# Kernel tuning notes

Hardware: AMD Instinct MI355X
Metric: run time of the kernel (lower is better)

Reference implementation:

```python
import jax, jax.numpy as jnp
import numpy as np

B, D, L = 2, 1024, 4096   # batch, channels (= num_heads), seq len
FS = 4                    # filter_size
DEPTH = 11                # ceil(log2((L-1)/(FS-1)+1))
LN_EPS = 1e-5


def setup_inputs() -> dict:
    key = jax.random.key(0)
    ks = jax.random.split(key, 7)
    return {
        "x": jax.random.normal(ks[0], (B, D, L), jnp.float32),
        "h0": jax.random.normal(ks[1], (D, 1, FS), jnp.float32) * 0.2,
        "h1": jax.random.normal(ks[2], (D, 1, FS), jnp.float32) * 0.2,
        "w_mix": jax.random.normal(ks[3], (D, D), jnp.float32) / np.sqrt(D),
        "b_mix": jnp.zeros((D,), jnp.float32),
        "ln_gamma": jnp.ones((D,), jnp.float32),
        "ln_beta": jnp.zeros((D,), jnp.float32),
    }


def _dw_conv(a, h, dilation):
    # depthwise (groups = D) dilated conv1d, cross-correlation like torch
    return jax.lax.conv_general_dilated(
        a, h, window_strides=(1,), padding='VALID',
        rhs_dilation=(dilation,),
        dimension_numbers=('NCH', 'OIH', 'NCH'),
        feature_group_count=D)


def reference(x, h0, h1, w_mix, b_mix, ln_gamma, ln_beta):
    # --- multires conv tree ---
    a = x
    dilation = 1
    a_list, b_list = [], []
    for _ in range(DEPTH):
        pad = dilation * (FS - 1)
        ap = jnp.pad(a, ((0, 0), (0, 0), (pad, 0)))  # left causal pad
        b = _dw_conv(ap, h1, dilation)
        a = _dw_conv(ap, h0, dilation)
        a_list.append(a)
        b_list.append(b)
        dilation *= 2
    # --- gated combination across scales (deepest level first) ---
    a_rev = a_list[::-1]
    b_rev = b_list[::-1]
    y = jnp.zeros_like(x)
    gated = None
    for i in range(DEPTH):
        if i + 1 < DEPTH:
            gated = jax.nn.sigmoid(a_rev[i]) * b_rev[i + 1]
        # last iteration reuses the previous gated tensor (matches original)
        y = y + gated
    # --- 1x1 channel mix (Dropout1d is identity in eval) + residual ---
    mixed = jnp.einsum('oc,bcl->bol', w_mix, y) + b_mix[None, :, None]
    z = mixed + x
    # --- LayerNorm over channel dim ---
    mu = jnp.mean(z, axis=1, keepdims=True)
    var = jnp.mean(jnp.square(z - mu), axis=1, keepdims=True)
    out = (z - mu) * jax.lax.rsqrt(var + LN_EPS)
    out = out * ln_gamma[None, :, None] + ln_beta[None, :, None]
    return out
```

## Files before the change

### kernel.cpp

```cpp
#include <hip/hip_runtime.h>
#include <hip/hip_bf16.h>

#define NB 2
#define ND 1024
#define NL 4096
#define NFS 4
#define NDEPTH 11
#define LN_EPS 1e-5f

#define BM 128
#define BN 128
#define BK 32
#define NKI (ND / BK)
#define ASZ (BM * BK)

#define CPAD 3072
#define CBUF (CPAD + NL)

typedef __bf16 bf16x8 __attribute__((ext_vector_type(8)));
typedef float f32x4 __attribute__((ext_vector_type(4)));

__device__ __forceinline__ unsigned short f2bf(float f) {
    __hip_bfloat16 h = __float2bfloat16(f);
    unsigned short u;
    __builtin_memcpy(&u, &h, 2);
    return u;
}

__device__ __forceinline__ float bf2f(unsigned short u) {
    unsigned int ui = (unsigned int)u << 16;
    float f;
    __builtin_memcpy(&f, &ui, 4);
    return f;
}

__device__ __forceinline__ unsigned int pack2bf(float lo, float hi) {
    return (unsigned int)f2bf(lo) | ((unsigned int)f2bf(hi) << 16);
}

__device__ __forceinline__ float sigm(float v) {
    return __builtin_amdgcn_rcpf(1.f + __expf(-v));
}

__device__ __forceinline__ void llds16(const void* g, void* l) {
    __builtin_amdgcn_global_load_lds(
        (const __attribute__((address_space(1))) unsigned int*)g,
        (__attribute__((address_space(3))) unsigned int*)l, 16, 0, 0);
}

__global__ __launch_bounds__(256) void wconv_kernel(const float* __restrict__ w,
                                                    unsigned short* __restrict__ wbf) {
    const int idx8 = (blockIdx.x * 256 + threadIdx.x) * 8;
    const float4 v0 = *reinterpret_cast<const float4*>(w + idx8);
    const float4 v1 = *reinterpret_cast<const float4*>(w + idx8 + 4);
    uint4 o;
    o.x = pack2bf(v0.x, v0.y);
    o.y = pack2bf(v0.z, v0.w);
    o.z = pack2bf(v1.x, v1.y);
    o.w = pack2bf(v1.z, v1.w);
    *reinterpret_cast<uint4*>(wbf + idx8) = o;
}

__global__ __launch_bounds__(512, 8) void conv_cascade_kernel(const float* __restrict__ x,
                                                              const float* __restrict__ h0,
                                                              const float* __restrict__ h1,
                                                              unsigned short* __restrict__ ybf) {
    __shared__ float a_sh[CBUF];
    const int row = blockIdx.x;
    const int d = row & (ND - 1);
    const int t = threadIdx.x;

#pragma unroll
    for (int i = 0; i < CPAD / 512; ++i) a_sh[i * 512 + t] = 0.f;

    const float* xrow = x + (size_t)row * NL;

    float h0c[NFS], h1c[NFS];
#pragma unroll
    for (int k = 0; k < NFS; ++k) {
        h0c[k] = h0[d * NFS + k];
        h1c[k] = h1[d * NFS + k];
    }

    float cur[2][4], yacc[2][4], bprev[2][4];
#pragma unroll
    for (int c = 0; c < 2; ++c) {
        const float4 v = *reinterpret_cast<const float4*>(xrow + c * 2048 + t * 4);
        cur[c][0] = v.x; cur[c][1] = v.y; cur[c][2] = v.z; cur[c][3] = v.w;
        *reinterpret_cast<float4*>(&a_sh[CPAD + c * 2048 + t * 4]) = v;
#pragma unroll
        for (int j = 0; j < 4; ++j) { yacc[c][j] = 0.f; bprev[c][j] = 0.f; }
    }
    __syncthreads();

#define CONV_MATH(c, A1, A2, A3, an, bn)                                             \
    _Pragma("unroll") for (int j = 0; j < 4; ++j) {                                  \
        an[j] = h0c[3] * cur[c][j] + h0c[2] * (A1)[j] + h0c[1] * (A2)[j] +           \
                h0c[0] * (A3)[j];                                                    \
        bn[j] = h1c[3] * cur[c][j] + h1c[2] * (A1)[j] + h1c[1] * (A2)[j] +           \
                h1c[0] * (A3)[j];                                                    \
    }
#define CONV_FIN(c, an, bn, SC)                                                      \
    {                                                                                \
        float4 wv; wv.x = an[0]; wv.y = an[1]; wv.z = an[2]; wv.w = an[3];           \
        *reinterpret_cast<float4*>(&a_sh[CPAD + (c)*2048 + t * 4]) = wv;             \
        if ((SC) > 0.f) {                                                            \
            _Pragma("unroll") for (int j = 0; j < 4; ++j)                            \
                yacc[c][j] += (SC)*sigm(an[j]) * bprev[c][j];                        \
        }                                                                            \
        _Pragma("unroll") for (int j = 0; j < 4; ++j) {                              \
            cur[c][j] = an[j];                                                       \
            bprev[c][j] = bn[j];                                                     \
        }                                                                            \
    }

    float an0[4], bn0[4], an1[4], bn1[4];

    {
        {
            const int A = CPAD + 0 * 2048 + t * 4;
            const float4 m1 = *reinterpret_cast<const float4*>(&a_sh[A - 4]);
            const float a1[4] = {m1.w, cur[0][0], cur[0][1], cur[0][2]};
            const float a2[4] = {m1.z, m1.w, cur[0][0], cur[0][1]};
            const float a3[4] = {m1.y, m1.z, m1.w, cur[0][0]};
            CONV_MATH(0, a1, a2, a3, an0, bn0)
        }
        {
            const int A = CPAD + 1 * 2048 + t * 4;
            const float4 m1 = *reinterpret_cast<const float4*>(&a_sh[A - 4]);
            const float a1[4] = {m1.w, cur[1][0], cur[1][1], cur[1][2]};
            const float a2[4] = {m1.z, m1.w, cur[1][0], cur[1][1]};
            const float a3[4] = {m1.y, m1.z, m1.w, cur[1][0]};
            CONV_MATH(1, a1, a2, a3, an1, bn1)
        }
        __syncthreads();
        CONV_FIN(0, an0, bn0, 0.f)
        CONV_FIN(1, an1, bn1, 0.f)
        __syncthreads();
    }

    {
        {
            const int A = CPAD + 0 * 2048 + t * 4;
            const float4 m1 = *reinterpret_cast<const float4*>(&a_sh[A - 4]);
            const float4 m2 = *reinterpret_cast<const float4*>(&a_sh[A - 8]);
            const float a1[4] = {m1.z, m1.w, cur[0][0], cur[0][1]};
            const float a2[4] = {m1.x, m1.y, m1.z, m1.w};
            const float a3[4] = {m2.z, m2.w, m1.x, m1.y};
            CONV_MATH(0, a1, a2, a3, an0, bn0)
        }
        {
            const int A = CPAD + 1 * 2048 + t * 4;
            const float4 m1 = *reinterpret_cast<const float4*>(&a_sh[A - 4]);
            const float4 m2 = *reinterpret_cast<const float4*>(&a_sh[A - 8]);
            const float a1[4] = {m1.z, m1.w, cur[1][0], cur[1][1]};
            const float a2[4] = {m1.x, m1.y, m1.z, m1.w};
            const float a3[4] = {m2.z, m2.w, m1.x, m1.y};
            CONV_MATH(1, a1, a2, a3, an1, bn1)
        }
        __syncthreads();
        CONV_FIN(0, an0, bn0, 2.f)
        CONV_FIN(1, an1, bn1, 2.f)
        __syncthreads();
    }

    int dil = 4;
#pragma unroll 1
    for (int lev = 2; lev <= 9; ++lev) {
        {
            const int A = CPAD + 0 * 2048 + t * 4;
            const float4 b1 = *reinterpret_cast<const float4*>(&a_sh[A - dil]);
            const float4 b2 = *reinterpret_cast<const float4*>(&a_sh[A - 2 * dil]);
            const float4 b3 = *reinterpret_cast<const float4*>(&a_sh[A - 3 * dil]);
            const float a1[4] = {b1.x, b1.y, b1.z, b1.w};
            const float a2[4] = {b2.x, b2.y, b2.z, b2.w};
            const float a3[4] = {b3.x, b3.y, b3.z, b3.w};
            CONV_MATH(0, a1, a2, a3, an0, bn0)
        }
        {
            const int A = CPAD + 1 * 2048 + t * 4;
            const float4 b1 = *reinterpret_cast<const float4*>(&a_sh[A - dil]);
            const float4 b2 = *reinterpret_cast<const float4*>(&a_sh[A - 2 * dil]);
            const float4 b3 = *reinterpret_cast<const float4*>(&a_sh[A - 3 * dil]);
            const float a1[4] = {b1.x, b1.y, b1.z, b1.w};
            const float a2[4] = {b2.x, b2.y, b2.z, b2.w};
            const float a3[4] = {b3.x, b3.y, b3.z, b3.w};
            CONV_MATH(1, a1, a2, a3, an1, bn1)
        }
        __syncthreads();
        CONV_FIN(0, an0, bn0, 1.f)
        CONV_FIN(1, an1, bn1, 1.f)
        dil <<= 1;
        __syncthreads();
    }

#pragma unroll
    for (int c = 0; c < 2; ++c) {
        const int A = CPAD + c * 2048 + t * 4;
        const float4 b1 = *reinterpret_cast<const float4*>(&a_sh[A - 1024]);
        const float4 b3 = *reinterpret_cast<const float4*>(&a_sh[A - 3072]);
#pragma unroll
        for (int j = 0; j < 4; ++j) {
            const float a1 = (&b1.x)[j];
            const float a2 = (c == 1) ? cur[0][j] : 0.f;
            const float a3 = (&b3.x)[j];
            const float an = h0c[3] * cur[c][j] + h0c[2] * a1 + h0c[1] * a2 + h0c[0] * a3;
            yacc[c][j] += sigm(an) * bprev[c][j];
        }
    }
#undef CONV_MATH
#undef CONV_FIN

#pragma unroll
    for (int c = 0; c < 2; ++c) {
        ushort4 o;
        o.x = f2bf(yacc[c][0]);
        o.y = f2bf(yacc[c][1]);
        o.z = f2bf(yacc[c][2]);
        o.w = f2bf(yacc[c][3]);
        *reinterpret_cast<ushort4*>(ybf + (size_t)row * NL + c * 2048 + t * 4) = o;
    }
}

__global__ __launch_bounds__(256) void transpose_kernel(const unsigned short* __restrict__ ybf,
                                                        unsigned short* __restrict__ yT) {
    __shared__ unsigned short tile[64][66];
    const int l0 = blockIdx.x * 64;
    const int c0 = blockIdx.y * 64;
    const int b = blockIdx.z;
    const int t = threadIdx.x;
    const int li = t & 63, cg = t >> 6;
#pragma unroll
    for (int k = 0; k < 16; ++k) {
        const int ci = cg * 16 + k;
        tile[ci][li] = ybf[(size_t)(b * ND + c0 + ci) * NL + l0 + li];
    }
    __syncthreads();
    const int ci2 = t & 63, lg = t >> 6;
#pragma unroll
    for (int k = 0; k < 16; ++k) {
        const int li2 = lg * 16 + k;
        yT[((size_t)b * NL + l0 + li2) * ND + c0 + ci2] = tile[ci2][li2];
    }
}

__global__ __launch_bounds__(256) void gemm_kernel(const unsigned short* __restrict__ wbf,
                                                   const unsigned short* __restrict__ yT,
                                                   const float* __restrict__ bmix,
                                                   unsigned short* __restrict__ mixed) {
    __shared__ unsigned short As[3][BM][BK];
    __shared__ unsigned short Bs[3][BN][BK];

    const int n0 = blockIdx.x * BN;
    const int m0 = blockIdx.y * BM;
    const int b = blockIdx.z;
    const int t = threadIdx.x;
    const int lane = t & 63, wid = t >> 6;
    const int wr = wid >> 1, wc = wid & 1;
    const int fr = lane & 15;
    const int fk = (lane >> 4) * 8;

    const int srow = wid * 32 + (lane >> 2);
    const int sk = (lane & 3) * 8;
    const unsigned short* Ag = wbf + (size_t)(m0 + srow) * ND + sk;
    const unsigned short* Bg = yT + ((size_t)b * NL + n0 + srow) * ND + sk;
    unsigned short* A0 = &As[0][0][0];
    unsigned short* B0 = &Bs[0][0][0];
    unsigned short* AsW = A0 + wid * 32 * BK;
    unsigned short* BsW = B0 + wid * 32 * BK;

#define STAGE(bo, kt)                           \
    llds16(Ag + (kt), AsW + (bo));              \
    llds16(Ag + (kt) + 16 * ND, AsW + (bo) + 16 * BK); \
    llds16(Bg + (kt), BsW + (bo));              \
    llds16(Bg + (kt) + 16 * ND, BsW + (bo) + 16 * BK);

    f32x4 acc[4][4];
#pragma unroll
    for (int mi = 0; mi < 4; ++mi)
#pragma unroll
        for (int ni = 0; ni < 4; ++ni)
            acc[mi][ni] = (f32x4){0.f, 0.f, 0.f, 0.f};

    STAGE(0, 0)
    STAGE(ASZ, BK)

    int bc = 0;
    int bs = 2;
#pragma unroll 1
    for (int ki = 0; ki < NKI; ++ki) {
        if (ki + 1 < NKI) {
            asm volatile("s_waitcnt vmcnt(4)" ::: "memory");
        } else {
            asm volatile("s_waitcnt vmcnt(0)" ::: "memory");
        }
        __builtin_amdgcn_s_barrier();
        __builtin_amdgcn_sched_barrier(0);

        if (ki + 2 < NKI) {
            const int bo = bs * ASZ;
            const int kt = (ki + 2) * BK;
            STAGE(bo, kt)
        }

        const int bco = bc * ASZ;
        bf16x8 af[4], bv[4];
#pragma unroll
        for (int mi = 0; mi < 4; ++mi)
            af[mi] = *reinterpret_cast<const bf16x8*>(A0 + bco + (wr * 64 + mi * 16 + fr) * BK + fk);
#pragma unroll
        for (int ni = 0; ni < 4; ++ni)
            bv[ni] = *reinterpret_cast<const bf16x8*>(B0 + bco + (wc * 64 + ni * 16 + fr) * BK + fk);
#pragma unroll
        for (int mi = 0; mi < 4; ++mi)
#pragma unroll
            for (int ni = 0; ni < 4; ++ni)
                acc[mi][ni] = __builtin_amdgcn_mfma_f32_16x16x32_bf16(af[mi], bv[ni],
                                                                      acc[mi][ni], 0, 0, 0);
        bc = (bc == 2) ? 0 : bc + 1;
        bs = (bs == 2) ? 0 : bs + 1;
    }
#undef STAGE

    const size_t bbase = (size_t)b * ND * NL;
#pragma unroll
    for (int mi = 0; mi < 4; ++mi) {
#pragma unroll
        for (int r = 0; r < 4; ++r) {
            const int o = m0 + wr * 64 + mi * 16 + (lane >> 4) * 4 + r;
            const float bm = bmix[o];
            const size_t rowbase = bbase + (size_t)o * NL;
#pragma unroll
            for (int ni = 0; ni < 4; ++ni) {
                const int l = n0 + wc * 64 + ni * 16 + fr;
                mixed[rowbase + l] = f2bf(acc[mi][ni][r] + bm);
            }
        }
    }
}

__global__ __launch_bounds__(512) void ln_kernel(const unsigned short* __restrict__ mixed,
                                                 const float* __restrict__ x,
                                                 const float* __restrict__ gamma,
                                                 const float* __restrict__ beta,
                                                 float* __restrict__ out) {
    const int b = blockIdx.y;
    const int l0 = blockIdx.x * 32;
    const int tl = threadIdx.x & 31, tg = threadIdx.x >> 5;
    const size_t base = (size_t)b * ND * NL + l0 + tl;

    float zv[64];
    float s = 0.f, q = 0.f;
#pragma unroll
    for (int j = 0; j < 64; ++j) {
        const size_t idx = base + (size_t)(tg + j * 16) * NL;
        const float v = bf2f(mixed[idx]) + x[idx];
        zv[j] = v;
        s += v;
        q += v * v;
    }

    __shared__ float sred[16][33], qred[16][33];
    __shared__ float mu_s[32], rs_s[32];
    sred[tg][tl] = s;
    qred[tg][tl] = q;
    __syncthreads();
    if (tg == 0) {
        float S = 0.f, Q = 0.f;
#pragma unroll
        for (int g = 0; g < 16; ++g) {
            S += sred[g][tl];
            Q += qred[g][tl];
        }
        const float mu = S * (1.f / ND);
        const float var = Q * (1.f / ND) - mu * mu;
        mu_s[tl] = mu;
        rs_s[tl] = rsqrtf(var + LN_EPS);
    }
    __syncthreads();
    const float mu = mu_s[tl], rs = rs_s[tl];
#pragma unroll
    for (int j = 0; j < 64; ++j) {
        const int c = tg + j * 16;
        out[base + (size_t)c * NL] = (zv[j] - mu) * rs * gamma[c] + beta[c];
    }
}

extern "C" void kernel_launch(void* const* d_in, const int* in_sizes, int n_in,
                              void* d_out, int out_size, void* d_ws, size_t ws_size,
                              hipStream_t stream) {
    (void)in_sizes; (void)n_in; (void)out_size; (void)ws_size;
    const float* x = (const float*)d_in[0];
    const float* h0 = (const float*)d_in[1];
    const float* h1 = (const float*)d_in[2];
    const float* wmix = (const float*)d_in[3];
    const float* bmix = (const float*)d_in[4];
    const float* gamma = (const float*)d_in[5];
    const float* beta = (const float*)d_in[6];
    float* out = (float*)d_out;

    char* ws = (char*)d_ws;
    unsigned short* ybf = (unsigned short*)(ws);
    unsigned short* yT = (unsigned short*)(ws + (size_t)16 * 1024 * 1024);
    unsigned short* wbf = (unsigned short*)(ws + (size_t)32 * 1024 * 1024);
    unsigned short* mixed = (unsigned short*)(ws + (size_t)34 * 1024 * 1024);

    wconv_kernel<<<dim3(ND * ND / (256 * 8)), 256, 0, stream>>>(wmix, wbf);
    conv_cascade_kernel<<<dim3(NB * ND), 512, 0, stream>>>(x, h0, h1, ybf);
    transpose_kernel<<<dim3(NL / 64, ND / 64, NB), 256, 0, stream>>>(ybf, yT);
    gemm_kernel<<<dim3(NL / BN, ND / BM, NB), 256, 0, stream>>>(wbf, yT, bmix, mixed);
    ln_kernel<<<dim3(NL / 32, NB), 512, 0, stream>>>(mixed, x, gamma, beta, out);
}
```

Measured before the change: 104.2 us.

## Run conv cascade in fp16 with packed half8 math and halved LDS

The depthwise conv cascade now keeps activations in LDS and registers as _Float16 and computes the filter taps with packed half8 vector arithmetic. Each thread handles 8 contiguous elements instead of two chunks of 4. The aim is to halve shared-memory footprint and traffic, use packed fp16 FMAs, and raise occupancy. The risk is fp16 range and precision loss over 11 cascaded levels, since values could grow or lose accuracy relative to the fp32 reference.

Result: no change. 105.2 us (+1.0%).

```diff
diff --git a/kernel.cpp b/kernel.cpp
--- a/kernel.cpp
+++ b/kernel.cpp
@@ -19,6 +19,7 @@
 
 typedef __bf16 bf16x8 __attribute__((ext_vector_type(8)));
 typedef float f32x4 __attribute__((ext_vector_type(4)));
+typedef _Float16 half8 __attribute__((ext_vector_type(8)));
 
 __device__ __forceinline__ unsigned short f2bf(float f) {
     __hip_bfloat16 h = __float2bfloat16(f);
@@ -65,161 +66,122 @@
                                                               const float* __restrict__ h0,
                                                               const float* __restrict__ h1,
                                                               unsigned short* __restrict__ ybf) {
-    __shared__ float a_sh[CBUF];
+    __shared__ _Float16 a_sh[CBUF];
     const int row = blockIdx.x;
     const int d = row & (ND - 1);
     const int t = threadIdx.x;
 
-#pragma unroll
-    for (int i = 0; i < CPAD / 512; ++i) a_sh[i * 512 + t] = 0.f;
+    if (t < CPAD / 8) *reinterpret_cast<half8*>(&a_sh[t * 8]) = (half8)0;
 
     const float* xrow = x + (size_t)row * NL;
 
-    float h0c[NFS], h1c[NFS];
+    _Float16 h0c[NFS], h1c[NFS];
 #pragma unroll
     for (int k = 0; k < NFS; ++k) {
-        h0c[k] = h0[d * NFS + k];
-        h1c[k] = h1[d * NFS + k];
-    }
-
-    float cur[2][4], yacc[2][4], bprev[2][4];
-#pragma unroll
-    for (int c = 0; c < 2; ++c) {
-        const float4 v = *reinterpret_cast<const float4*>(xrow + c * 2048 + t * 4);
-        cur[c][0] = v.x; cur[c][1] = v.y; cur[c][2] = v.z; cur[c][3] = v.w;
-        *reinterpret_cast<float4*>(&a_sh[CPAD + c * 2048 + t * 4]) = v;
-#pragma unroll
-        for (int j = 0; j < 4; ++j) { yacc[c][j] = 0.f; bprev[c][j] = 0.f; }
-    }
+        h0c[k] = (_Float16)h0[d * NFS + k];
+        h1c[k] = (_Float16)h1[d * NFS + k];
+    }
+
+    half8 cur;
+    {
+        const float4 v0 = *reinterpret_cast<const float4*>(xrow + t * 8);
+        const float4 v1 = *reinterpret_cast<const float4*>(xrow + t * 8 + 4);
+        cur[0] = (_Float16)v0.x; cur[1] = (_Float16)v0.y;
+        cur[2] = (_Float16)v0.z; cur[3] = (_Float16)v0.w;
+        cur[4] = (_Float16)v1.x; cur[5] = (_Float16)v1.y;
+        cur[6] = (_Float16)v1.z; cur[7] = (_Float16)v1.w;
+    }
+    const int A = CPAD + t * 8;
+    *reinterpret_cast<half8*>(&a_sh[A]) = cur;
+
+    float yacc[8];
+    half8 bprev = (half8)0;
+#pragma unroll
+    for (int j = 0; j < 8; ++j) yacc[j] = 0.f;
     __syncthreads();
 
-#define CONV_MATH(c, A1, A2, A3, an, bn)                                             \
-    _Pragma("unroll") for (int j = 0; j < 4; ++j) {                                  \
-        an[j] = h0c[3] * cur[c][j] + h0c[2] * (A1)[j] + h0c[1] * (A2)[j] +           \
-                h0c[0] * (A3)[j];                                                    \
-        bn[j] = h1c[3] * cur[c][j] + h1c[2] * (A1)[j] + h1c[1] * (A2)[j] +           \
-                h1c[0] * (A3)[j];                                                    \
-    }
-#define CONV_FIN(c, an, bn, SC)                                                      \
-    {                                                                                \
-        float4 wv; wv.x = an[0]; wv.y = an[1]; wv.z = an[2]; wv.w = an[3];           \
-        *reinterpret_cast<float4*>(&a_sh[CPAD + (c)*2048 + t * 4]) = wv;             \
-        if ((SC) > 0.f) {                                                            \
-            _Pragma("unroll") for (int j = 0; j < 4; ++j)                            \
-                yacc[c][j] += (SC)*sigm(an[j]) * bprev[c][j];                        \
-        }                                                                            \
-        _Pragma("unroll") for (int j = 0; j < 4; ++j) {                              \
-            cur[c][j] = an[j];                                                       \
-            bprev[c][j] = bn[j];                                                     \
-        }                                                                            \
-    }
-
-    float an0[4], bn0[4], an1[4], bn1[4];
-
-    {
-        {
-            const int A = CPAD + 0 * 2048 + t * 4;
-            const float4 m1 = *reinterpret_cast<const float4*>(&a_sh[A - 4]);
-            const float a1[4] = {m1.w, cur[0][0], cur[0][1], cur[0][2]};
-            const float a2[4] = {m1.z, m1.w, cur[0][0], cur[0][1]};
-            const float a3[4] = {m1.y, m1.z, m1.w, cur[0][0]};
-            CONV_MATH(0, a1, a2, a3, an0, bn0)
-        }
-        {
-            const int A = CPAD + 1 * 2048 + t * 4;
-            const float4 m1 = *reinterpret_cast<const float4*>(&a_sh[A - 4]);
-            const float a1[4] = {m1.w, cur[1][0], cur[1][1], cur[1][2]};
-            const float a2[4] = {m1.z, m1.w, cur[1][0], cur[1][1]};
-            const float a3[4] = {m1.y, m1.z, m1.w, cur[1][0]};
-            CONV_MATH(1, a1, a2, a3, an1, bn1)
-        }
-        __syncthreads();
-        CONV_FIN(0, an0, bn0, 0.f)
-        CONV_FIN(1, an1, bn1, 0.f)
-        __syncthreads();
-    }
-
-    {
-        {
-            const int A = CPAD + 0 * 2048 + t * 4;
-            const float4 m1 = *reinterpret_cast<const float4*>(&a_sh[A - 4]);
-            const float4 m2 = *reinterpret_cast<const float4*>(&a_sh[A - 8]);
-            const float a1[4] = {m1.z, m1.w, cur[0][0], cur[0][1]};
-            const float a2[4] = {m1.x, m1.y, m1.z, m1.w};
-            const float a3[4] = {m2.z, m2.w, m1.x, m1.y};
-            CONV_MATH(0, a1, a2, a3, an0, bn0)
-        }
-        {
-            const int A = CPAD + 1 * 2048 + t * 4;
-            const float4 m1 = *reinterpret_cast<const float4*>(&a_sh[A - 4]);
-            const float4 m2 = *reinterpret_cast<const float4*>(&a_sh[A - 8]);
-            const float a1[4] = {m1.z, m1.w, cur[1][0], cur[1][1]};
-            const float a2[4] = {m1.x, m1.y, m1.z, m1.w};
-            const float a3[4] = {m2.z, m2.w, m1.x, m1.y};
-            CONV_MATH(1, a1, a2, a3, an1, bn1)
-        }
-        __syncthreads();
-        CONV_FIN(0, an0, bn0, 2.f)
-        CONV_FIN(1, an1, bn1, 2.f)
-        __syncthreads();
-    }
-
-    int dil = 4;
+    half8 an, bn;
+
+#define CONV_MATH(a1, a2, a3)                                       \
+    an = cur * h0c[3] + (a1)*h0c[2] + (a2)*h0c[1] + (a3)*h0c[0];    \
+    bn = cur * h1c[3] + (a1)*h1c[2] + (a2)*h1c[1] + (a3)*h1c[0];
+
+#define CONV_FIN(SC)                                                \
+    {                                                               \
+        *reinterpret_cast<half8*>(&a_sh[A]) = an;                   \
+        if ((SC) > 0.f) {                                           \
+            _Pragma("unroll") for (int j = 0; j < 8; ++j)           \
+                yacc[j] += (SC)*sigm((float)an[j]) * (float)bprev[j]; \
+        }                                                           \
+        cur = an;                                                   \
+        bprev = bn;                                                 \
+    }
+
+    {
+        const half8 m = *reinterpret_cast<const half8*>(&a_sh[A - 8]);
+        const half8 a1 = __builtin_shufflevector(m, cur, 7, 8, 9, 10, 11, 12, 13, 14);
+        const half8 a2 = __builtin_shufflevector(m, cur, 6, 7, 8, 9, 10, 11, 12, 13);
+        const half8 a3 = __builtin_shufflevector(m, cur, 5, 6, 7, 8, 9, 10, 11, 12);
+        CONV_MATH(a1, a2, a3)
+        __syncthreads();
+        CONV_FIN(0.f)
+        __syncthreads();
+    }
+
+    {
+        const half8 m = *reinterpret_cast<const half8*>(&a_sh[A - 8]);
+        const half8 a1 = __builtin_shufflevector(m, cur, 6, 7, 8, 9, 10, 11, 12, 13);
+        const half8 a2 = __builtin_shufflevector(m, cur, 4, 5, 6, 7, 8, 9, 10, 11);
+        const half8 a3 = __builtin_shufflevector(m, cur, 2, 3, 4, 5, 6, 7, 8, 9);
+        CONV_MATH(a1, a2, a3)
+        __syncthreads();
+        CONV_FIN(2.f)
+        __syncthreads();
+    }
+
+    {
+        const half8 m = *reinterpret_cast<const half8*>(&a_sh[A - 8]);
+        const half8 m2 = *reinterpret_cast<const half8*>(&a_sh[A - 16]);
+        const half8 a1 = __builtin_shufflevector(m, cur, 4, 5, 6, 7, 8, 9, 10, 11);
+        const half8 a2 = m;
+        const half8 a3 = __builtin_shufflevector(m2, m, 4, 5, 6, 7, 8, 9, 10, 11);
+        CONV_MATH(a1, a2, a3)
+        __syncthreads();
+        CONV_FIN(1.f)
+        __syncthreads();
+    }
+
+    int dil = 8;
 #pragma unroll 1
-    for (int lev = 2; lev <= 9; ++lev) {
-        {
-            const int A = CPAD + 0 * 2048 + t * 4;
-            const float4 b1 = *reinterpret_cast<const float4*>(&a_sh[A - dil]);
-            const float4 b2 = *reinterpret_cast<const float4*>(&a_sh[A - 2 * dil]);
-            const float4 b3 = *reinterpret_cast<const float4*>(&a_sh[A - 3 * dil]);
-            const float a1[4] = {b1.x, b1.y, b1.z, b1.w};
-            const float a2[4] = {b2.x, b2.y, b2.z, b2.w};
-            const float a3[4] = {b3.x, b3.y, b3.z, b3.w};
-            CONV_MATH(0, a1, a2, a3, an0, bn0)
-        }
-        {
-            const int A = CPAD + 1 * 2048 + t * 4;
-            const float4 b1 = *reinterpret_cast<const float4*>(&a_sh[A - dil]);
-            const float4 b2 = *reinterpret_cast<const float4*>(&a_sh[A - 2 * dil]);
-            const float4 b3 = *reinterpret_cast<const float4*>(&a_sh[A - 3 * dil]);
-            const float a1[4] = {b1.x, b1.y, b1.z, b1.w};
-            const float a2[4] = {b2.x, b2.y, b2.z, b2.w};
-            const float a3[4] = {b3.x, b3.y, b3.z, b3.w};
-            CONV_MATH(1, a1, a2, a3, an1, bn1)
-        }
-        __syncthreads();
-        CONV_FIN(0, an0, bn0, 1.f)
-        CONV_FIN(1, an1, bn1, 1.f)
+    for (int lev = 3; lev <= 9; ++lev) {
+        const half8 a1 = *reinterpret_cast<const half8*>(&a_sh[A - dil]);
+        const half8 a2 = *reinterpret_cast<const half8*>(&a_sh[A - 2 * dil]);
+        const half8 a3 = *reinterpret_cast<const half8*>(&a_sh[A - 3 * dil]);
+        CONV_MATH(a1, a2, a3)
+        __syncthreads();
+        CONV_FIN(1.f)
         dil <<= 1;
         __syncthreads();
     }
 
-#pragma unroll
-    for (int c = 0; c < 2; ++c) {
-        const int A = CPAD + c * 2048 + t * 4;
-        const float4 b1 = *reinterpret_cast<const float4*>(&a_sh[A - 1024]);
-        const float4 b3 = *reinterpret_cast<const float4*>(&a_sh[A - 3072]);
-#pragma unroll
-        for (int j = 0; j < 4; ++j) {
-            const float a1 = (&b1.x)[j];
-            const float a2 = (c == 1) ? cur[0][j] : 0.f;
-            const float a3 = (&b3.x)[j];
-            const float an = h0c[3] * cur[c][j] + h0c[2] * a1 + h0c[1] * a2 + h0c[0] * a3;
-            yacc[c][j] += sigm(an) * bprev[c][j];
-        }
+    {
+        const half8 a1 = *reinterpret_cast<const half8*>(&a_sh[A - 1024]);
+        const half8 a2 = *reinterpret_cast<const half8*>(&a_sh[A - 2048]);
+        const half8 a3 = *reinterpret_cast<const half8*>(&a_sh[A - 3072]);
+        an = cur * h0c[3] + a1 * h0c[2] + a2 * h0c[1] + a3 * h0c[0];
+#pragma unroll
+        for (int j = 0; j < 8; ++j)
+            yacc[j] += sigm((float)an[j]) * (float)bprev[j];
     }
 #undef CONV_MATH
 #undef CONV_FIN
 
-#pragma unroll
-    for (int c = 0; c < 2; ++c) {
-        ushort4 o;
-        o.x = f2bf(yacc[c][0]);
-        o.y = f2bf(yacc[c][1]);
-        o.z = f2bf(yacc[c][2]);
-        o.w = f2bf(yacc[c][3]);
-        *reinterpret_cast<ushort4*>(ybf + (size_t)row * NL + c * 2048 + t * 4) = o;
-    }
+    uint4 o;
+    o.x = pack2bf(yacc[0], yacc[1]);
+    o.y = pack2bf(yacc[2], yacc[3]);
+    o.z = pack2bf(yacc[4], yacc[5]);
+    o.w = pack2bf(yacc[6], yacc[7]);
+    *reinterpret_cast<uint4*>(ybf + (size_t)row * NL + t * 8) = o;
 }
 
 __global__ __launch_bounds__(256) void transpose_kernel(const unsigned short* __restrict__ ybf,
```
